# Performance work log

Hardware: AMD Instinct MI355X
Metric: run time of the kernel (lower is better)

## Reference

```python
import jax, jax.numpy as jnp
import numpy as np

N_NODES = 50000
N_EDGES = 800000
D = 128
H = 8
HD = D // H
N_NTYPES = 3
N_ETYPES = 5
LN_EPS = 1e-5


def setup_inputs() -> dict:
    key = jax.random.key(0)
    ks = jax.random.split(key, 16)
    inp = {
        "x": jax.random.normal(ks[0], (N_NODES, D), dtype=jnp.float32),
        "edge_index": jax.random.randint(ks[1], (2, N_EDGES), 0, N_NODES),
        "edge_type": jax.random.randint(ks[2], (N_EDGES,), 0, N_ETYPES),
        "node_type": jax.random.randint(ks[3], (N_NODES,), 0, N_NTYPES),
        # per-(node_type, head) QKV projections, per-(edge_type, head) K transform
        "W_Q": jax.random.normal(ks[4], (N_NTYPES, H, HD, HD), dtype=jnp.float32) * 0.02,
        "W_K": jax.random.normal(ks[5], (N_NTYPES, H, HD, HD), dtype=jnp.float32) * 0.02,
        "W_V": jax.random.normal(ks[6], (N_NTYPES, H, HD, HD), dtype=jnp.float32) * 0.02,
        "W_edge": jax.random.normal(ks[7], (N_ETYPES, H, HD, HD), dtype=jnp.float32) * 0.02,
        "mu": jnp.ones((H, N_ETYPES), dtype=jnp.float32),
        "W_out": jax.random.normal(ks[8], (D, D), dtype=jnp.float32) * 0.02,
        "b_out": jnp.zeros((D,), dtype=jnp.float32),
        "ln1_g": jnp.ones((D,), dtype=jnp.float32),
        "ln1_b": jnp.zeros((D,), dtype=jnp.float32),
        "W1": jax.random.normal(ks[9], (D, 4 * D), dtype=jnp.float32) * 0.02,
        "b1": jnp.zeros((4 * D,), dtype=jnp.float32),
        "W2": jax.random.normal(ks[10], (4 * D, D), dtype=jnp.float32) * 0.02,
        "b2": jnp.zeros((D,), dtype=jnp.float32),
        "ln2_g": jnp.ones((D,), dtype=jnp.float32),
        "ln2_b": jnp.zeros((D,), dtype=jnp.float32),
    }
    return inp


def _layer_norm(y, g, b):
    m = y.mean(-1, keepdims=True)
    v = ((y - m) ** 2).mean(-1, keepdims=True)
    return (y - m) * jax.lax.rsqrt(v + LN_EPS) * g + b


def reference(x, edge_index, edge_type, node_type,
              W_Q, W_K, W_V, W_edge, mu,
              W_out, b_out, ln1_g, ln1_b, W1, b1, W2, b2, ln2_g, ln2_b):
    N = x.shape[0]
    xh = x.reshape(N, H, HD)  # heads vectorized (concat of per-head slices)

    # type-specific QKV: small fixed loop over node types, masked select
    Q = jnp.zeros_like(xh)
    K = jnp.zeros_like(xh)
    V = jnp.zeros_like(xh)
    for t in range(N_NTYPES):
        m = (node_type == t)[:, None, None]
        Q = jnp.where(m, jnp.einsum('nhd,hdf->nhf', xh, W_Q[t]), Q)
        K = jnp.where(m, jnp.einsum('nhd,hdf->nhf', xh, W_K[t]), K)
        V = jnp.where(m, jnp.einsum('nhd,hdf->nhf', xh, W_V[t]), V)

    src, dst = edge_index[0], edge_index[1]
    q_dst = Q[dst]   # [E,H,HD]
    k_src = K[src]   # [E,H,HD]

    # edge-type-specific K transform
    kt = jnp.zeros_like(k_src)
    for et in range(N_ETYPES):
        m = (edge_type == et)[:, None, None]
        kt = jnp.where(m, jnp.einsum('ehd,hdf->ehf', k_src, W_edge[et]), kt)

    scores = (q_dst * kt).sum(-1) / jnp.sqrt(jnp.float32(HD))  # [E,H]
    scores = scores * mu[:, edge_type].T                       # mu per edge type, per head

    # sparse softmax over incoming edges of each dst node, per head
    smax = jax.ops.segment_max(scores, dst, num_segments=N)
    ex = jnp.exp(scores - smax[dst])
    den = jax.ops.segment_sum(ex, dst, num_segments=N)
    w = ex / (den[dst] + 1e-10)                                 # [E,H]

    agg = jax.ops.segment_sum(V[src] * w[..., None], dst, num_segments=N)  # [N,H,HD]
    mh = agg.reshape(N, D) @ W_out + b_out  # dropout is identity in eval

    h = _layer_norm(x + mh, ln1_g, ln1_b)
    ffn = jax.nn.gelu(h @ W1 + b1, approximate=False) @ W2 + b2
    return _layer_norm(h + ffn, ln2_g, ln2_b)
```

## Files before the change

### kernel.cpp

```cpp
#include <hip/hip_runtime.h>
#include <hip/hip_bf16.h>

#define N_NODESC 50000
#define N_EDGESC 800000
#define DD 128
#define HH 8
#define HDIM 16
#define N_NT 3
#define N_ET 5
#define NPB 196
#define NEB 400
#define NFB 512

#define KV8_OFF    ((size_t)0)
#define QT8_OFF    ((size_t)12800000)
#define XP_OFF     ((size_t)44800000)
#define AGG_OFF    ((size_t)57600000)
#define WOUTT_OFF  ((size_t)83200000)
#define W1T_OFF    ((size_t)83232768)
#define W2T_OFF    ((size_t)83363840)
#define WALL_OFF   ((size_t)83494912)
#define EDATA_OFF  ((size_t)84183040)
#define ROWS_OFF   ((size_t)87383040)
#define ORIG_OFF   ((size_t)87583104)
#define DEG_OFF    ((size_t)87783104)
#define TOFS_OFF   ((size_t)87983104)
#define BH_OFF     ((size_t)87983168)
#define BB_OFF     ((size_t)87985536)
#define TMP_OFF    ((size_t)87988928)
#define RLOC_OFF   ((size_t)91188928)
#define CSUM_OFF   ((size_t)91389056)

using short8 = __attribute__((ext_vector_type(8))) short;
using f32x4  = __attribute__((ext_vector_type(4))) float;
using f32x2  = __attribute__((ext_vector_type(2))) float;

__device__ __forceinline__ ushort f2b(float f) {
    __hip_bfloat16 h = __float2bfloat16(f);
    return *(ushort*)&h;
}
__device__ __forceinline__ float b2f(ushort u) {
    __hip_bfloat16 h = *(__hip_bfloat16*)&u;
    return __bfloat162float(h);
}
__device__ __forceinline__ f32x2 pk0(unsigned int w) {
    return __builtin_amdgcn_cvt_pk_f32_fp8((int)w, false);
}
__device__ __forceinline__ f32x2 pk1(unsigned int w) {
    return __builtin_amdgcn_cvt_pk_f32_fp8((int)w, true);
}
__device__ __forceinline__ float gelu_f(float v) {
    const float x = v * 0.70710678118654752f;
    const float ax = fabsf(x);
    const float d = fmaf(0.3275911f, ax, 1.0f);
    float t;
    asm("v_rcp_f32 %0, %1" : "=v"(t) : "v"(d));
    float p = fmaf(1.061405429f, t, -1.453152027f);
    p = fmaf(p, t, 1.421413741f);
    p = fmaf(p, t, -0.284496736f);
    p = fmaf(p, t, 0.254829592f);
    p = p * t;
    const float e = __expf(-ax * ax);
    const float er = 1.0f - p * e;
    const float erfx = (x < 0.f) ? -er : er;
    return 0.5f * v * (1.0f + erfx);
}
__device__ __forceinline__ void ebar() {
    __builtin_amdgcn_sched_barrier(0);
    asm volatile("s_waitcnt lgkmcnt(0)" ::: "memory");
    __builtin_amdgcn_sched_barrier(0);
    __builtin_amdgcn_s_barrier();
    __builtin_amdgcn_sched_barrier(0);
}

__global__ __launch_bounds__(256) void prep_a(
    const float* __restrict__ Wout, const float* __restrict__ W1, const float* __restrict__ W2,
    const float* __restrict__ WQ, const float* __restrict__ Wk, const float* __restrict__ Wv,
    const float* __restrict__ We, const float* __restrict__ mu,
    ushort* __restrict__ Woutt, ushort* __restrict__ W1t, ushort* __restrict__ W2t,
    ushort* __restrict__ Wall,
    const int* __restrict__ ntype, int* __restrict__ bh,
    const int* __restrict__ dst, int* __restrict__ deg, unsigned int* __restrict__ tmp)
{
    const int b = blockIdx.x, tid = threadIdx.x;
    if (b < 1920) {
        const int gid = b * 256 + tid;
        if (gid < 16384) {
            const int nn = gid >> 7, k = gid & 127;
            Woutt[gid] = f2b(Wout[k * 128 + nn]);
        } else if (gid < 81920) {
            const int i = gid - 16384;
            const int nn = i >> 7, k = i & 127;
            W1t[i] = f2b(W1[k * 512 + nn]);
        } else if (gid < 147456) {
            const int i = gid - 81920;
            const int nn = i >> 9, k = i & 511;
            W2t[i] = f2b(W2[k * 128 + nn]);
        } else {
            const int idx = gid - 147456;
            const int t = idx / (896 * 128);
            const int rem = idx % (896 * 128);
            const int c = rem / 128, k = rem % 128;
            const int hk = k >> 4, ck = k & 15;
            float v = 0.f;
            if (c < 128) {
                const int hc = c >> 4, j = c & 15;
                if (hk == hc) v = 4.f * Wk[((t * HH + hc) * HDIM + ck) * HDIM + j];
            } else if (c < 256) {
                const int c2 = c - 128, hc = c2 >> 4, j = c2 & 15;
                if (hk == hc) v = 4.f * Wv[((t * HH + hc) * HDIM + ck) * HDIM + j];
            } else {
                const int cq = c - 256, et = cq >> 7, dd = cq & 127;
                const int hq = dd >> 4, j = dd & 15;
                if (hk == hq) {
                    const float* wq = WQ + ((t * HH + hq) * HDIM + ck) * HDIM;
                    const float* we = We + ((et * HH + hq) * HDIM + j) * HDIM;
                    float s = 0.f;
#pragma unroll
                    for (int f = 0; f < 16; f++) s = fmaf(wq[f], we[f], s);
                    v = 64.f * mu[hq * N_ET + et] * s;
                }
            }
            Wall[idx] = f2b(v);
        }
    } else if (b < 1920 + NPB) {
        const int bc = b - 1920;
        const int wave = tid >> 6, lane = tid & 63;
        const int n = bc * 256 + tid;
        const int t = (n < N_NODESC) ? ntype[n] : -1;
        const unsigned long long m0 = __ballot(t == 0);
        const unsigned long long m1 = __ballot(t == 1);
        const unsigned long long m2 = __ballot(t == 2);
        __shared__ int wcnt[4][3];
        if (lane == 0) {
            wcnt[wave][0] = (int)__popcll(m0);
            wcnt[wave][1] = (int)__popcll(m1);
            wcnt[wave][2] = (int)__popcll(m2);
        }
        __syncthreads();
        if (tid < 3)
            bh[tid * NPB + bc] = wcnt[0][tid] + wcnt[1][tid] + wcnt[2][tid] + wcnt[3][tid];
    } else {
        for (int e = (b - 1920 - NPB) * 256 + tid; e < N_EDGESC; e += NEB * 256) {
            const int nd = dst[e];
            const unsigned int p = (unsigned int)atomicAdd(&deg[nd], 1);
            tmp[e] = (p << 16) | (unsigned int)nd;
        }
    }
}

__global__ __launch_bounds__(256) void prep_b(
    const int* __restrict__ bh, const int* __restrict__ deg,
    int* __restrict__ bb, int* __restrict__ tofs,
    int* __restrict__ rloc, int* __restrict__ csum)
{
    __shared__ int part[256];
    const int tid = threadIdx.x;
    if (blockIdx.x == 0) {
        const int base3 = tid * 3;
        int e0 = (base3 + 0 < 588) ? bh[base3 + 0] : 0;
        int e1 = (base3 + 1 < 588) ? bh[base3 + 1] : 0;
        int e2 = (base3 + 2 < 588) ? bh[base3 + 2] : 0;
        const int l0 = e0, l1 = e0 + e1, l2 = l1 + e2;
        part[tid] = l2;
        __syncthreads();
        for (int off = 1; off < 256; off <<= 1) {
            const int u = (tid >= off) ? part[tid - off] : 0;
            __syncthreads();
            part[tid] += u;
            __syncthreads();
        }
        const int tb = part[tid] - l2;
        if (base3 + 0 < 588) bb[base3 + 0] = tb;
        if (base3 + 1 < 588) bb[base3 + 1] = tb + l0;
        if (base3 + 2 < 588) bb[base3 + 2] = tb + l1;
        __syncthreads();
        if (tid == 0) {
            tofs[0] = 0;
            tofs[1] = bb[NPB];
            tofs[2] = bb[2 * NPB];
            tofs[3] = N_NODESC;
        }
    } else {
        const int c = blockIdx.x - 1;
        const int n = c * 256 + tid;
        const int vdeg = (n < N_NODESC) ? deg[n] : 0;
        part[tid] = vdeg;
        __syncthreads();
        for (int off = 1; off < 256; off <<= 1) {
            const int u = (tid >= off) ? part[tid - off] : 0;
            __syncthreads();
            part[tid] += u;
            __syncthreads();
        }
        if (n <= N_NODESC) rloc[n] = part[tid] - vdeg;
        if (tid == 255) csum[c] = part[255];
    }
}

__global__ __launch_bounds__(256) void prep_c(
    const int* __restrict__ ntype, const float* __restrict__ x,
    const int* __restrict__ src, const int* __restrict__ etype,
    const int* __restrict__ bb, const int* __restrict__ rloc, const int* __restrict__ csum,
    const unsigned int* __restrict__ tmp,
    int* __restrict__ origof, ushort* __restrict__ Xp, int* __restrict__ rows,
    int* __restrict__ edata)
{
    const int b = blockIdx.x, tid = threadIdx.x;
    __shared__ int cb[256];
    {
        const int v = (tid < NPB) ? csum[tid] : 0;
        cb[tid] = v;
        __syncthreads();
        for (int off = 1; off < 256; off <<= 1) {
            const int u = (tid >= off) ? cb[tid - off] : 0;
            __syncthreads();
            cb[tid] += u;
            __syncthreads();
        }
        const int incl = cb[tid];
        __syncthreads();
        cb[tid] = incl - v;
        __syncthreads();
    }

    if (b < NPB) {
        const int wave = tid >> 6, lane = tid & 63;
        const int n = b * 256 + tid;
        const int t = (n < N_NODESC) ? ntype[n] : -1;
        const unsigned long long m0 = __ballot(t == 0);
        const unsigned long long m1 = __ballot(t == 1);
        const unsigned long long m2 = __ballot(t == 2);
        __shared__ int wcnt[4][3];
        __shared__ int sp[256];
        if (lane == 0) {
            wcnt[wave][0] = (int)__popcll(m0);
            wcnt[wave][1] = (int)__popcll(m1);
            wcnt[wave][2] = (int)__popcll(m2);
        }
        __syncthreads();
        int p = -1;
        if (n < N_NODESC) {
            int basew = 0;
#pragma unroll
            for (int w = 0; w < 4; w++) if (w < wave) basew += wcnt[w][t];
            const unsigned long long mt = (t == 0) ? m0 : (t == 1) ? m1 : m2;
            const unsigned long long mlt = ((unsigned long long)1 << lane) - 1;
            p = bb[t * NPB + b] + basew + (int)__popcll(mt & mlt);
            origof[p] = n;
        }
        if (n <= N_NODESC) rows[n] = cb[b] + rloc[n];
        sp[tid] = p;
        __syncthreads();
        for (int i = tid; i < 256 * 16; i += 256) {
            const int nn = i >> 4, c = (i & 15) << 3;
            const int pp = sp[nn];
            if (pp < 0) continue;
            const int n2 = b * 256 + nn;
            const float4 v0 = *(const float4*)(x + (size_t)n2 * DD + c);
            const float4 v1 = *(const float4*)(x + (size_t)n2 * DD + c + 4);
            ushort o[8] = {f2b(v0.x), f2b(v0.y), f2b(v0.z), f2b(v0.w),
                           f2b(v1.x), f2b(v1.y), f2b(v1.z), f2b(v1.w)};
            *(uint4*)(Xp + (size_t)pp * DD + c) = *(uint4*)o;
        }
    } else {
        for (int e = (b - NPB) * 256 + tid; e < N_EDGESC; e += NFB * 256) {
            const unsigned int v = tmp[e];
            const int nd = (int)(v & 0xffffu);
            const int p = (int)(v >> 16);
            edata[cb[nd >> 8] + rloc[nd] + p] = src[e] | (etype[e] << 16);
        }
    }
}

#define LDP 36

__global__ __launch_bounds__(256) void proj_gemm(
    const ushort* __restrict__ Xp, const ushort* __restrict__ Wall,
    const int* __restrict__ tofs, const int* __restrict__ origof,
    ushort* __restrict__ KV8, unsigned char* __restrict__ Qt8)
{
    const int t = blockIdx.z;
    const int rs = tofs[t], re = tofs[t + 1];
    const int mBase = rs + blockIdx.x * 128;
    if (mBase >= re) return;
    const int nBase = blockIdx.y * 128;
    const ushort* Bt = Wall + (size_t)t * 896 * 128;

    __shared__ ushort As[128 * LDP];
    __shared__ ushort Bs[128 * LDP];
    const int tid = threadIdx.x;
    const int lane = tid & 63, wave = tid >> 6;
    const int mw = (wave >> 1) * 64, nw = (wave & 1) * 64;
    const int l15 = lane & 15, q8 = (lane >> 4) * 8;

    f32x4 acc[4][4];
#pragma unroll
    for (int i = 0; i < 4; i++)
#pragma unroll
        for (int j = 0; j < 4; j++) acc[i][j] = (f32x4){0.f, 0.f, 0.f, 0.f};

    const int r0 = tid >> 2, c0 = (tid & 3) * 8;
    int rA0 = mBase + r0;      if (rA0 >= N_NODESC) rA0 = N_NODESC - 1;
    int rA1 = mBase + r0 + 64; if (rA1 >= N_NODESC) rA1 = N_NODESC - 1;

    for (int kk = 0; kk < 128; kk += 32) {
        short8 a0 = *(const short8*)(Xp + (size_t)rA0 * DD + kk + c0);
        short8 a1 = *(const short8*)(Xp + (size_t)rA1 * DD + kk + c0);
        short8 b0 = *(const short8*)(Bt + (size_t)(nBase + r0) * 128 + kk + c0);
        short8 b1 = *(const short8*)(Bt + (size_t)(nBase + r0 + 64) * 128 + kk + c0);
        *(short8*)&As[r0 * LDP + c0] = a0;
        *(short8*)&As[(r0 + 64) * LDP + c0] = a1;
        *(short8*)&Bs[r0 * LDP + c0] = b0;
        *(short8*)&Bs[(r0 + 64) * LDP + c0] = b1;
        __syncthreads();
        short8 af[4], bf[4];
#pragma unroll
        for (int i = 0; i < 4; i++)
            af[i] = *(const short8*)&As[(mw + i * 16 + l15) * LDP + q8];
#pragma unroll
        for (int j = 0; j < 4; j++)
            bf[j] = *(const short8*)&Bs[(nw + j * 16 + l15) * LDP + q8];
#pragma unroll
        for (int i = 0; i < 4; i++)
#pragma unroll
            for (int j = 0; j < 4; j++)
                acc[i][j] = __builtin_amdgcn_mfma_f32_16x16x32_bf16(af[i], bf[j], acc[i][j], 0, 0, 0);
        __syncthreads();
    }

    unsigned char* kvb = (unsigned char*)KV8;
    const int rq = (lane >> 4) * 4;
#pragma unroll
    for (int i = 0; i < 4; i++) {
#pragma unroll
        for (int r = 0; r < 4; r++) {
            const int gm = mBase + mw + i * 16 + rq + r;
            if (gm >= re) continue;
            const int og = origof[gm];
#pragma unroll
            for (int j = 0; j < 4; j++) {
                const int gn = nBase + nw + j * 16 + l15;
                const float v = acc[i][j][r];
                const unsigned char b8 =
                    (unsigned char)(__builtin_amdgcn_cvt_pk_fp8_f32(v, v, 0, false) & 0xff);
                if (gn < 256) kvb[(size_t)og * 256 + gn] = b8;
                else          Qt8[(size_t)og * 640 + (gn - 256)] = b8;
            }
        }
    }
}

__global__ __launch_bounds__(128) void edgeagg_kernel(
    const int* __restrict__ rowstart, const int* __restrict__ edata,
    const unsigned char* __restrict__ Qt8, const unsigned char* __restrict__ KV8,
    ushort* __restrict__ agg)
{
    const int w = threadIdx.x >> 6;
    const int lane = threadIdx.x & 63;
    const int n = blockIdx.x * 2 + w;
    const int slot = lane >> 3;
    const int h = lane & 7;

    __shared__ uint4 qs8s[2][40];
    if (lane < 40)
        qs8s[w][lane] = ((const uint4*)(Qt8 + (size_t)n * 640))[lane];
    __syncthreads();
    const uint* qbase = (const uint*)&qs8s[w][0];

    const int s0 = rowstart[n], s1 = rowstart[n + 1];
    const float qsc = 1.44269504f / 1024.f;

    float acc[16];
#pragma unroll
    for (int j = 0; j < 16; j++) acc[j] = 0.f;
    float den = 0.f;

    for (int i = s0 + slot; i < s1; i += 8) {
        const int ed = edata[i];
        const int sn = ed & 0xffff;
        const int et = ed >> 16;
        const unsigned char* kvp = KV8 + ((size_t)sn << 8);
        const uint4 kw = *(const uint4*)(kvp + (h << 4));
        const uint4 vw = *(const uint4*)(kvp + 128 + (h << 4));
        const uint4 qw = *(const uint4*)(qbase + (et << 5) + (h << 2));

        const f32x2 q0 = pk0(qw.x), q1 = pk1(qw.x), q2 = pk0(qw.y), q3 = pk1(qw.y);
        const f32x2 q4 = pk0(qw.z), q5 = pk1(qw.z), q6 = pk0(qw.w), q7 = pk1(qw.w);
        const f32x2 k0 = pk0(kw.x), k1 = pk1(kw.x), k2 = pk0(kw.y), k3 = pk1(kw.y);
        const f32x2 k4 = pk0(kw.z), k5 = pk1(kw.z), k6 = pk0(kw.w), k7 = pk1(kw.w);

        float pa = q0.x * k0.x;
        float pb = q0.y * k0.y;
        float pc = q1.x * k1.x;
        float pd = q1.y * k1.y;
        pa = fmaf(q2.x, k2.x, pa); pb = fmaf(q2.y, k2.y, pb);
        pc = fmaf(q3.x, k3.x, pc); pd = fmaf(q3.y, k3.y, pd);
        pa = fmaf(q4.x, k4.x, pa); pb = fmaf(q4.y, k4.y, pb);
        pc = fmaf(q5.x, k5.x, pc); pd = fmaf(q5.y, k5.y, pd);
        pa = fmaf(q6.x, k6.x, pa); pb = fmaf(q6.y, k6.y, pb);
        pc = fmaf(q7.x, k7.x, pc); pd = fmaf(q7.y, k7.y, pd);

        const float ex = exp2f(((pa + pb) + (pc + pd)) * qsc);
        den += ex;

        const f32x2 v0 = pk0(vw.x), v1 = pk1(vw.x), v2 = pk0(vw.y), v3 = pk1(vw.y);
        const f32x2 v4 = pk0(vw.z), v5 = pk1(vw.z), v6 = pk0(vw.w), v7 = pk1(vw.w);
        acc[0]  = fmaf(ex, v0.x, acc[0]);  acc[1]  = fmaf(ex, v0.y, acc[1]);
        acc[2]  = fmaf(ex, v1.x, acc[2]);  acc[3]  = fmaf(ex, v1.y, acc[3]);
        acc[4]  = fmaf(ex, v2.x, acc[4]);  acc[5]  = fmaf(ex, v2.y, acc[5]);
        acc[6]  = fmaf(ex, v3.x, acc[6]);  acc[7]  = fmaf(ex, v3.y, acc[7]);
        acc[8]  = fmaf(ex, v4.x, acc[8]);  acc[9]  = fmaf(ex, v4.y, acc[9]);
        acc[10] = fmaf(ex, v5.x, acc[10]); acc[11] = fmaf(ex, v5.y, acc[11]);
        acc[12] = fmaf(ex, v6.x, acc[12]); acc[13] = fmaf(ex, v6.y, acc[13]);
        acc[14] = fmaf(ex, v7.x, acc[14]); acc[15] = fmaf(ex, v7.y, acc[15]);
    }

    {
        const int b0 = slot & 1, b1 = slot & 2, b2 = slot & 4;
#pragma unroll
        for (int j = 0; j < 8; j++) {
            const float v = b0 ? acc[j] : acc[j + 8];
            const float r = __shfl_xor(v, 8);
            acc[j] = (b0 ? acc[j + 8] : acc[j]) + r;
        }
#pragma unroll
        for (int j = 0; j < 4; j++) {
            const float v = b1 ? acc[j] : acc[j + 4];
            const float r = __shfl_xor(v, 16);
            acc[j] = (b1 ? acc[j + 4] : acc[j]) + r;
        }
#pragma unroll
        for (int j = 0; j < 2; j++) {
            const float v = b2 ? acc[j] : acc[j + 2];
            const float r = __shfl_xor(v, 32);
            acc[j] = (b2 ? acc[j + 2] : acc[j]) + r;
        }
        den += __shfl_xor(den, 8);
        den += __shfl_xor(den, 16);
        den += __shfl_xor(den, 32);
    }
    const float rr = 0.25f / (den + 1e-10f);
    const int fb = (h << 4) + ((slot & 1) << 3) + ((slot & 2) << 1) + ((slot & 4) >> 1);
    ushort o2[2] = { f2b(acc[0] * rr), f2b(acc[1] * rr) };
    *(uint*)&agg[((size_t)n << 7) + fb] = *(uint*)o2;
}

#define LDH 132
#define LDB2 68

#define LOADB(P0, P1, PTR) { P0 = *(const short8*)(PTR); P1 = *(const short8*)((PTR) + 8); }
#define STAGEB(BUF, P0, P1) { *(short8*)&Bs[BUF][br * LDB2 + bc] = P0; \
                              *(short8*)&Bs[BUF][br * LDB2 + bc + 8] = P1; }

__global__ __launch_bounds__(512, 4) void fused_tail(
    const ushort* __restrict__ agg, const ushort* __restrict__ Woutt,
    const ushort* __restrict__ W1t, const ushort* __restrict__ W2t,
    const float* __restrict__ x,
    const float* __restrict__ bout, const float* __restrict__ g1, const float* __restrict__ b1ln,
    const float* __restrict__ b1, const float* __restrict__ b2,
    const float* __restrict__ g2, const float* __restrict__ b2ln,
    float* __restrict__ out)
{
    __shared__ ushort Bs[2][128 * LDB2];
    __shared__ ushort Hs[64 * LDH];
    __shared__ ushort Ts[64 * LDH];
    __shared__ float red[2][4][64];

    const int tid = threadIdx.x;
    const int lane = tid & 63, wave = tid >> 6;
    const int wm = wave >> 2, wn = wave & 3;
    const int l15 = lane & 15, q8 = (lane >> 4) * 8, rq = (lane >> 4) * 4;
    const int mBase = blockIdx.x * 64;

    const int br = tid >> 2, bc = (tid & 3) * 16;
    const int ar = tid >> 3, ac = (tid & 7) * 16;
    int rowA = mBase + ar; if (rowA >= N_NODESC) rowA = N_NODESC - 1;

    f32x4 acc1[2][2], acc2[2][2];
#pragma unroll
    for (int i = 0; i < 2; i++)
#pragma unroll
        for (int j = 0; j < 2; j++) {
            acc1[i][j] = (f32x4){0.f, 0.f, 0.f, 0.f};
            acc2[i][j] = (f32x4){0.f, 0.f, 0.f, 0.f};
        }

    short8 pX0, pX1, pY0, pY1, aT0, aT1;
    LOADB(pX0, pX1, Woutt + (size_t)br * 128 + bc);
    LOADB(pY0, pY1, Woutt + (size_t)br * 128 + 64 + bc);
    aT0 = *(const short8*)(agg + (size_t)rowA * DD + ac);
    aT1 = *(const short8*)(agg + (size_t)rowA * DD + ac + 8);
    float xv[2][4][2];
#pragma unroll
    for (int i = 0; i < 2; i++)
#pragma unroll
        for (int r = 0; r < 4; r++) {
            const int gm = mBase + wm * 32 + i * 16 + rq + r;
            const int gr = (gm < N_NODESC) ? gm : N_NODESC - 1;
#pragma unroll
            for (int j = 0; j < 2; j++)
                xv[i][r][j] = x[(size_t)gr * DD + wn * 32 + j * 16 + l15];
        }
    *(short8*)&Ts[ar * LDH + ac] = aT0;
    *(short8*)&Ts[ar * LDH + ac + 8] = aT1;
    STAGEB(0, pX0, pX1);
    LOADB(pX0, pX1, W1t + (size_t)br * 128 + bc);
    ebar();

    STAGEB(1, pY0, pY1);
    LOADB(pY0, pY1, W1t + (size_t)br * 128 + 64 + bc);
#pragma unroll
    for (int kk2 = 0; kk2 < 2; kk2++) {
        short8 af[2], bf[2];
#pragma unroll
        for (int i = 0; i < 2; i++)
            af[i] = *(const short8*)&Ts[(wm * 32 + i * 16 + l15) * LDH + kk2 * 32 + q8];
#pragma unroll
        for (int j = 0; j < 2; j++)
            bf[j] = *(const short8*)&Bs[0][(wn * 32 + j * 16 + l15) * LDB2 + kk2 * 32 + q8];
#pragma unroll
        for (int i = 0; i < 2; i++)
#pragma unroll
            for (int j = 0; j < 2; j++)
                acc1[i][j] = __builtin_amdgcn_mfma_f32_16x16x32_bf16(af[i], bf[j], acc1[i][j], 0, 0, 0);
    }
    ebar();

    STAGEB(0, pX0, pX1);
    LOADB(pX0, pX1, W2t + (size_t)br * 512 + bc);
#pragma unroll
    for (int kk2 = 0; kk2 < 2; kk2++) {
        short8 af[2], bf[2];
#pragma unroll
        for (int i = 0; i < 2; i++)
            af[i] = *(const short8*)&Ts[(wm * 32 + i * 16 + l15) * LDH + 64 + kk2 * 32 + q8];
#pragma unroll
        for (int j = 0; j < 2; j++)
            bf[j] = *(const short8*)&Bs[1][(wn * 32 + j * 16 + l15) * LDB2 + kk2 * 32 + q8];
#pragma unroll
        for (int i = 0; i < 2; i++)
#pragma unroll
            for (int j = 0; j < 2; j++)
                acc1[i][j] = __builtin_amdgcn_mfma_f32_16x16x32_bf16(af[i], bf[j], acc1[i][j], 0, 0, 0);
    }
    ebar();

    {
        float bo[2], gv[2], bv[2];
#pragma unroll
        for (int j = 0; j < 2; j++) {
            const int gn = wn * 32 + j * 16 + l15;
            bo[j] = bout[gn]; gv[j] = g1[gn]; bv[j] = b1ln[gn];
        }
#pragma unroll
        for (int i = 0; i < 2; i++) {
#pragma unroll
            for (int r = 0; r < 4; r++) {
                const int row = wm * 32 + i * 16 + rq + r;
                float s = 0.f, ss = 0.f;
#pragma unroll
                for (int j = 0; j < 2; j++) {
                    float v = acc1[i][j][r] + bo[j] + xv[i][r][j];
                    acc1[i][j][r] = v;
                    s += v; ss += v * v;
                }
                s  += __shfl_xor(s, 1);  s  += __shfl_xor(s, 2);  s  += __shfl_xor(s, 4);  s  += __shfl_xor(s, 8);
                ss += __shfl_xor(ss, 1); ss += __shfl_xor(ss, 2); ss += __shfl_xor(ss, 4); ss += __shfl_xor(ss, 8);
                if (l15 == 0) { red[0][wn][row] = s; red[1][wn][row] = ss; }
            }
        }
        ebar();
#pragma unroll
        for (int i = 0; i < 2; i++) {
#pragma unroll
            for (int r = 0; r < 4; r++) {
                const int row = wm * 32 + i * 16 + rq + r;
                const float s  = red[0][0][row] + red[0][1][row] + red[0][2][row] + red[0][3][row];
                const float ss = red[1][0][row] + red[1][1][row] + red[1][2][row] + red[1][3][row];
                const float mean = s * (1.f / 128.f);
                const float var  = ss * (1.f / 128.f) - mean * mean;
                const float rstd = rsqrtf(var + 1e-5f);
#pragma unroll
                for (int j = 0; j < 2; j++) {
                    const int gn = wn * 32 + j * 16 + l15;
                    Hs[row * LDH + gn] = f2b((acc1[i][j][r] - mean) * rstd * gv[j] + bv[j]);
                }
            }
// ... 102 lines not shown
                for (int j = 0; j < 2; j++)
                    acc2[i][j] = __builtin_amdgcn_mfma_f32_16x16x32_bf16(af[i], bf[j], acc2[i][j], 0, 0, 0);
        }
        ebar();
    }

    {
        float b2v[2], gv[2], bv[2];
#pragma unroll
        for (int j = 0; j < 2; j++) {
            const int gn = wn * 32 + j * 16 + l15;
            b2v[j] = b2[gn]; gv[j] = g2[gn]; bv[j] = b2ln[gn];
        }
#pragma unroll
        for (int i = 0; i < 2; i++) {
#pragma unroll
            for (int r = 0; r < 4; r++) {
                const int row = wm * 32 + i * 16 + rq + r;
                float s = 0.f, ss = 0.f;
#pragma unroll
                for (int j = 0; j < 2; j++) {
                    const int gn = wn * 32 + j * 16 + l15;
                    float v = acc2[i][j][r] + b2v[j] + b2f(Hs[row * LDH + gn]);
                    acc2[i][j][r] = v;
                    s += v; ss += v * v;
                }
                s  += __shfl_xor(s, 1);  s  += __shfl_xor(s, 2);  s  += __shfl_xor(s, 4);  s  += __shfl_xor(s, 8);
                ss += __shfl_xor(ss, 1); ss += __shfl_xor(ss, 2); ss += __shfl_xor(ss, 4); ss += __shfl_xor(ss, 8);
                if (l15 == 0) { red[0][wn][row] = s; red[1][wn][row] = ss; }
            }
        }
        ebar();
#pragma unroll
        for (int i = 0; i < 2; i++) {
#pragma unroll
            for (int r = 0; r < 4; r++) {
                const int row = wm * 32 + i * 16 + rq + r;
                const int gm = mBase + row;
                if (gm >= N_NODESC) continue;
                const float s  = red[0][0][row] + red[0][1][row] + red[0][2][row] + red[0][3][row];
                const float ss = red[1][0][row] + red[1][1][row] + red[1][2][row] + red[1][3][row];
                const float mean = s * (1.f / 128.f);
                const float var  = ss * (1.f / 128.f) - mean * mean;
                const float rstd = rsqrtf(var + 1e-5f);
#pragma unroll
                for (int j = 0; j < 2; j++) {
                    const int gn = wn * 32 + j * 16 + l15;
                    out[(size_t)gm * DD + gn] = (acc2[i][j][r] - mean) * rstd * gv[j] + bv[j];
                }
            }
        }
    }
}

extern "C" void kernel_launch(void* const* d_in, const int* in_sizes, int n_in,
                              void* d_out, int out_size, void* d_ws, size_t ws_size,
                              hipStream_t stream)
{
    const float* x     = (const float*)d_in[0];
    const int*   ei    = (const int*)d_in[1];
    const int*   etyp  = (const int*)d_in[2];
    const int*   ntype = (const int*)d_in[3];
    const float* Wq    = (const float*)d_in[4];
    const float* Wk    = (const float*)d_in[5];
    const float* Wv    = (const float*)d_in[6];
    const float* We    = (const float*)d_in[7];
    const float* mu    = (const float*)d_in[8];
    const float* Wout  = (const float*)d_in[9];
    const float* bout  = (const float*)d_in[10];
    const float* g1    = (const float*)d_in[11];
    const float* b1ln  = (const float*)d_in[12];
    const float* W1    = (const float*)d_in[13];
    const float* b1    = (const float*)d_in[14];
    const float* W2    = (const float*)d_in[15];
    const float* b2    = (const float*)d_in[16];
    const float* g2    = (const float*)d_in[17];
    const float* b2ln  = (const float*)d_in[18];
    float* out = (float*)d_out;

    char* ws = (char*)d_ws;
    ushort*        KV8   = (ushort*)(ws + KV8_OFF);
    unsigned char* Qt8   = (unsigned char*)(ws + QT8_OFF);
    ushort*        Xp    = (ushort*)(ws + XP_OFF);
    ushort*        agg   = (ushort*)(ws + AGG_OFF);
    ushort*        Woutt = (ushort*)(ws + WOUTT_OFF);
    ushort*        W1t   = (ushort*)(ws + W1T_OFF);
    ushort*        W2t   = (ushort*)(ws + W2T_OFF);
    ushort*        Wall  = (ushort*)(ws + WALL_OFF);
    int*           edata = (int*)(ws + EDATA_OFF);
    int*           rows  = (int*)(ws + ROWS_OFF);
    int*           origof= (int*)(ws + ORIG_OFF);
    int*           deg   = (int*)(ws + DEG_OFF);
    int*           tofs  = (int*)(ws + TOFS_OFF);
    int*           bh    = (int*)(ws + BH_OFF);
    int*           bb    = (int*)(ws + BB_OFF);
    unsigned int*  tmp   = (unsigned int*)(ws + TMP_OFF);
    int*           rloc  = (int*)(ws + RLOC_OFF);
    int*           csum  = (int*)(ws + CSUM_OFF);

    const int* srcA = ei;
    const int* dstA = ei + N_EDGESC;

    (void)hipMemsetAsync(ws + DEG_OFF, 0, 200000, stream);

    prep_a<<<1920 + NPB + NEB, 256, 0, stream>>>(
        Wout, W1, W2, Wq, Wk, Wv, We, mu, Woutt, W1t, W2t, Wall,
        ntype, bh, dstA, deg, tmp);
    prep_b<<<1 + NPB, 256, 0, stream>>>(bh, deg, bb, tofs, rloc, csum);
    prep_c<<<NPB + NFB, 256, 0, stream>>>(ntype, x, srcA, etyp, bb, rloc, csum, tmp,
                                          origof, Xp, rows, edata);

    proj_gemm<<<dim3(394, 7, 3), 256, 0, stream>>>(Xp, Wall, tofs, origof, KV8, Qt8);
    edgeagg_kernel<<<N_NODESC / 2, 128, 0, stream>>>(rows, edata, Qt8,
                                                     (const unsigned char*)KV8, agg);

    fused_tail<<<782, 512, 0, stream>>>(agg, Woutt, W1t, W2t, x,
                                        bout, g1, b1ln, b1, b2, g2, b2ln, out);
}
```

Measured before the change: 322.3 us.

## Fuse edge attention aggregation into the tail GEMM kernel

Removes the separate edge aggregation kernel and performs the per-node sparse softmax aggregation inside fused_tail. Each wave processes 8 consecutive nodes, double-buffering their Q vectors in shared memory, and writes the aggregated result straight into the shared A tile. This drops the global round trip for agg and one kernel launch. In exchange, each wave handles nodes serially inside a block sized for the GEMM (782 blocks), so gather parallelism and latency hiding may drop compared with the 25000-block standalone kernel.

```diff
diff --git a/kernel.cpp b/kernel.cpp
--- a/kernel.cpp
+++ b/kernel.cpp
@@ -15,7 +15,6 @@
 #define KV8_OFF    ((size_t)0)
 #define QT8_OFF    ((size_t)12800000)
 #define XP_OFF     ((size_t)44800000)
-#define AGG_OFF    ((size_t)57600000)
 #define WOUTT_OFF  ((size_t)83200000)
 #define W1T_OFF    ((size_t)83232768)
 #define W2T_OFF    ((size_t)83363840)
@@ -351,101 +350,6 @@
     }
 }
 
-__global__ __launch_bounds__(128) void edgeagg_kernel(
-    const int* __restrict__ rowstart, const int* __restrict__ edata,
-    const unsigned char* __restrict__ Qt8, const unsigned char* __restrict__ KV8,
-    ushort* __restrict__ agg)
-{
-    const int w = threadIdx.x >> 6;
-    const int lane = threadIdx.x & 63;
-    const int n = blockIdx.x * 2 + w;
-    const int slot = lane >> 3;
-    const int h = lane & 7;
-
-    __shared__ uint4 qs8s[2][40];
-    if (lane < 40)
-        qs8s[w][lane] = ((const uint4*)(Qt8 + (size_t)n * 640))[lane];
-    __syncthreads();
-    const uint* qbase = (const uint*)&qs8s[w][0];
-
-    const int s0 = rowstart[n], s1 = rowstart[n + 1];
-    const float qsc = 1.44269504f / 1024.f;
-
-    float acc[16];
-#pragma unroll
-    for (int j = 0; j < 16; j++) acc[j] = 0.f;
-    float den = 0.f;
-
-    for (int i = s0 + slot; i < s1; i += 8) {
-        const int ed = edata[i];
-        const int sn = ed & 0xffff;
-        const int et = ed >> 16;
-        const unsigned char* kvp = KV8 + ((size_t)sn << 8);
-        const uint4 kw = *(const uint4*)(kvp + (h << 4));
-        const uint4 vw = *(const uint4*)(kvp + 128 + (h << 4));
-        const uint4 qw = *(const uint4*)(qbase + (et << 5) + (h << 2));
-
-        const f32x2 q0 = pk0(qw.x), q1 = pk1(qw.x), q2 = pk0(qw.y), q3 = pk1(qw.y);
-        const f32x2 q4 = pk0(qw.z), q5 = pk1(qw.z), q6 = pk0(qw.w), q7 = pk1(qw.w);
-        const f32x2 k0 = pk0(kw.x), k1 = pk1(kw.x), k2 = pk0(kw.y), k3 = pk1(kw.y);
-        const f32x2 k4 = pk0(kw.z), k5 = pk1(kw.z), k6 = pk0(kw.w), k7 = pk1(kw.w);
-
-        float pa = q0.x * k0.x;
-        float pb = q0.y * k0.y;
-        float pc = q1.x * k1.x;
-        float pd = q1.y * k1.y;
-        pa = fmaf(q2.x, k2.x, pa); pb = fmaf(q2.y, k2.y, pb);
-        pc = fmaf(q3.x, k3.x, pc); pd = fmaf(q3.y, k3.y, pd);
-        pa = fmaf(q4.x, k4.x, pa); pb = fmaf(q4.y, k4.y, pb);
-        pc = fmaf(q5.x, k5.x, pc); pd = fmaf(q5.y, k5.y, pd);
-        pa = fmaf(q6.x, k6.x, pa); pb = fmaf(q6.y, k6.y, pb);
-        pc = fmaf(q7.x, k7.x, pc); pd = fmaf(q7.y, k7.y, pd);
-
-        const float ex = exp2f(((pa + pb) + (pc + pd)) * qsc);
-        den += ex;
-
-        const f32x2 v0 = pk0(vw.x), v1 = pk1(vw.x), v2 = pk0(vw.y), v3 = pk1(vw.y);
-        const f32x2 v4 = pk0(vw.z), v5 = pk1(vw.z), v6 = pk0(vw.w), v7 = pk1(vw.w);
-        acc[0]  = fmaf(ex, v0.x, acc[0]);  acc[1]  = fmaf(ex, v0.y, acc[1]);
-        acc[2]  = fmaf(ex, v1.x, acc[2]);  acc[3]  = fmaf(ex, v1.y, acc[3]);
-        acc[4]  = fmaf(ex, v2.x, acc[4]);  acc[5]  = fmaf(ex, v2.y, acc[5]);
-        acc[6]  = fmaf(ex, v3.x, acc[6]);  acc[7]  = fmaf(ex, v3.y, acc[7]);
-        acc[8]  = fmaf(ex, v4.x, acc[8]);  acc[9]  = fmaf(ex, v4.y, acc[9]);
-        acc[10] = fmaf(ex, v5.x, acc[10]); acc[11] = fmaf(ex, v5.y, acc[11]);
-        acc[12] = fmaf(ex, v6.x, acc[12]); acc[13] = fmaf(ex, v6.y, acc[13]);
-        acc[14] = fmaf(ex, v7.x, acc[14]); acc[15] = fmaf(ex, v7.y, acc[15]);
-    }
-
-    {
-        const int b0 = slot & 1, b1 = slot & 2, b2 = slot & 4;
-#pragma unroll
-        for (int j = 0; j < 8; j++) {
-            const float v = b0 ? acc[j] : acc[j + 8];
-            const float r = __shfl_xor(v, 8);
-            acc[j] = (b0 ? acc[j + 8] : acc[j]) + r;
-        }
-#pragma unroll
-        for (int j = 0; j < 4; j++) {
-            const float v = b1 ? acc[j] : acc[j + 4];
-            const float r = __shfl_xor(v, 16);
-            acc[j] = (b1 ? acc[j + 4] : acc[j]) + r;
-        }
-#pragma unroll
-        for (int j = 0; j < 2; j++) {
-            const float v = b2 ? acc[j] : acc[j + 2];
-            const float r = __shfl_xor(v, 32);
-            acc[j] = (b2 ? acc[j + 2] : acc[j]) + r;
-        }
-        den += __shfl_xor(den, 8);
-        den += __shfl_xor(den, 16);
-        den += __shfl_xor(den, 32);
-    }
-    const float rr = 0.25f / (den + 1e-10f);
-    const int fb = (h << 4) + ((slot & 1) << 3) + ((slot & 2) << 1) + ((slot & 4) >> 1);
-    ushort o2[2] = { f2b(acc[0] * rr), f2b(acc[1] * rr) };
-    *(uint*)&agg[((size_t)n << 7) + fb] = *(uint*)o2;
-}
-
 #define LDH 132
 #define LDB2 68
 
@@ -454,17 +358,19 @@
                               *(short8*)&Bs[BUF][br * LDB2 + bc + 8] = P1; }
 
 __global__ __launch_bounds__(512, 4) void fused_tail(
-    const ushort* __restrict__ agg, const ushort* __restrict__ Woutt,
-    const ushort* __restrict__ W1t, const ushort* __restrict__ W2t,
+    const int* __restrict__ rows, const int* __restrict__ edata,
+    const unsigned char* __restrict__ Qt8, const unsigned char* __restrict__ KV8,
+    const ushort* __restrict__ Woutt, const ushort* __restrict__ W1t,
+    const ushort* __restrict__ W2t,
     const float* __restrict__ x,
     const float* __restrict__ bout, const float* __restrict__ g1, const float* __restrict__ b1ln,
     const float* __restrict__ b1, const float* __restrict__ b2,
     const float* __restrict__ g2, const float* __restrict__ b2ln,
     float* __restrict__ out)
 {
-    __shared__ ushort Bs[2][128 * LDB2];
-    __shared__ ushort Hs[64 * LDH];
-    __shared__ ushort Ts[64 * LDH];
+    __shared__ __align__(16) ushort Bs[2][128 * LDB2];
+    __shared__ __align__(16) ushort Hs[64 * LDH];
+    __shared__ __align__(16) ushort Ts[64 * LDH];
     __shared__ float red[2][4][64];
 
     const int tid = threadIdx.x;
@@ -474,8 +380,120 @@
     const int mBase = blockIdx.x * 64;
 
     const int br = tid >> 2, bc = (tid & 3) * 16;
-    const int ar = tid >> 3, ac = (tid & 7) * 16;
-    int rowA = mBase + ar; if (rowA >= N_NODESC) rowA = N_NODESC - 1;
+
+    short8 pX0, pX1, pY0, pY1;
+    LOADB(pX0, pX1, Woutt + (size_t)br * 128 + bc);
+    LOADB(pY0, pY1, Woutt + (size_t)br * 128 + 64 + bc);
+    float xv[2][4][2];
+#pragma unroll
+    for (int i = 0; i < 2; i++)
+#pragma unroll
+        for (int r = 0; r < 4; r++) {
+            const int gm = mBase + wm * 32 + i * 16 + rq + r;
+            const int gr = (gm < N_NODESC) ? gm : N_NODESC - 1;
+#pragma unroll
+            for (int j = 0; j < 2; j++)
+                xv[i][r][j] = x[(size_t)gr * DD + wn * 32 + j * 16 + l15];
+        }
+
+    {
+        const int slot = lane >> 3;
+        const int h = lane & 7;
+        uint* Hqu = (uint*)Hs;
+        const int qbA = wave * 320, qbB = qbA + 160;
+        {
+            const int nd0 = mBase + wave * 8;
+            if (lane < 40 && nd0 < N_NODESC)
+                *(uint4*)&Hqu[qbA + lane * 4] =
+                    ((const uint4*)(Qt8 + (size_t)nd0 * 640))[lane];
+        }
+        const float qsc = 1.44269504f / 1024.f;
+        for (int q = 0; q < 8; q++) {
+            const int nd = mBase + wave * 8 + q;
+            uint4 nq = make_uint4(0u, 0u, 0u, 0u);
+            if (q < 7 && lane < 40 && nd + 1 < N_NODESC)
+                nq = ((const uint4*)(Qt8 + (size_t)(nd + 1) * 640))[lane];
+            if (nd < N_NODESC) {
+                const uint* qbase = &Hqu[(q & 1) ? qbB : qbA];
+                const int s0 = rows[nd], s1 = rows[nd + 1];
+                float acc[16];
+#pragma unroll
+                for (int j = 0; j < 16; j++) acc[j] = 0.f;
+                float den = 0.f;
+                for (int i = s0 + slot; i < s1; i += 8) {
+                    const int ed = edata[i];
+                    const int sn = ed & 0xffff;
+                    const int et = ed >> 16;
+                    const unsigned char* kvp = KV8 + ((size_t)sn << 8);
+                    const uint4 kw = *(const uint4*)(kvp + (h << 4));
+                    const uint4 vw = *(const uint4*)(kvp + 128 + (h << 4));
+                    const uint4 qw = *(const uint4*)(qbase + (et << 5) + (h << 2));
+
+                    const f32x2 q0 = pk0(qw.x), q1 = pk1(qw.x), q2 = pk0(qw.y), q3 = pk1(qw.y);
+                    const f32x2 q4 = pk0(qw.z), q5 = pk1(qw.z), q6 = pk0(qw.w), q7 = pk1(qw.w);
+                    const f32x2 k0 = pk0(kw.x), k1 = pk1(kw.x), k2 = pk0(kw.y), k3 = pk1(kw.y);
+                    const f32x2 k4 = pk0(kw.z), k5 = pk1(kw.z), k6 = pk0(kw.w), k7 = pk1(kw.w);
+
+                    float pa = q0.x * k0.x;
+                    float pb = q0.y * k0.y;
+                    float pc = q1.x * k1.x;
+                    float pd = q1.y * k1.y;
+                    pa = fmaf(q2.x, k2.x, pa); pb = fmaf(q2.y, k2.y, pb);
+                    pc = fmaf(q3.x, k3.x, pc); pd = fmaf(q3.y, k3.y, pd);
+                    pa = fmaf(q4.x, k4.x, pa); pb = fmaf(q4.y, k4.y, pb);
+                    pc = fmaf(q5.x, k5.x, pc); pd = fmaf(q5.y, k5.y, pd);
+                    pa = fmaf(q6.x, k6.x, pa); pb = fmaf(q6.y, k6.y, pb);
+                    pc = fmaf(q7.x, k7.x, pc); pd = fmaf(q7.y, k7.y, pd);
+
+                    const float ex = exp2f(((pa + pb) + (pc + pd)) * qsc);
+                    den += ex;
+
+                    const f32x2 v0 = pk0(vw.x), v1 = pk1(vw.x), v2 = pk0(vw.y), v3 = pk1(vw.y);
+                    const f32x2 v4 = pk0(vw.z), v5 = pk1(vw.z), v6 = pk0(vw.w), v7 = pk1(vw.w);
+                    acc[0]  = fmaf(ex, v0.x, acc[0]);  acc[1]  = fmaf(ex, v0.y, acc[1]);
+                    acc[2]  = fmaf(ex, v1.x, acc[2]);  acc[3]  = fmaf(ex, v1.y, acc[3]);
+                    acc[4]  = fmaf(ex, v2.x, acc[4]);  acc[5]  = fmaf(ex, v2.y, acc[5]);
+                    acc[6]  = fmaf(ex, v3.x, acc[6]);  acc[7]  = fmaf(ex, v3.y, acc[7]);
+                    acc[8]  = fmaf(ex, v4.x, acc[8]);  acc[9]  = fmaf(ex, v4.y, acc[9]);
+                    acc[10] = fmaf(ex, v5.x, acc[10]); acc[11] = fmaf(ex, v5.y, acc[11]);
+                    acc[12] = fmaf(ex, v6.x, acc[12]); acc[13] = fmaf(ex, v6.y, acc[13]);
+                    acc[14] = fmaf(ex, v7.x, acc[14]); acc[15] = fmaf(ex, v7.y, acc[15]);
+                }
+                {
+                    const int b0 = slot & 1, b1s = slot & 2, b2s = slot & 4;
+#pragma unroll
+                    for (int j = 0; j < 8; j++) {
+                        const float v = b0 ? acc[j] : acc[j + 8];
+                        const float r = __shfl_xor(v, 8);
+                        acc[j] = (b0 ? acc[j + 8] : acc[j]) + r;
+                    }
+#pragma unroll
+                    for (int j = 0; j < 4; j++) {
+                        const float v = b1s ? acc[j] : acc[j + 4];
+                        const float r = __shfl_xor(v, 16);
+                        acc[j] = (b1s ? acc[j + 4] : acc[j]) + r;
+                    }
+#pragma unroll
+                    for (int j = 0; j < 2; j++) {
+                        const float v = b2s ? acc[j] : acc[j + 2];
+                        const float r = __shfl_xor(v, 32);
+                        acc[j] = (b2s ? acc[j + 2] : acc[j]) + r;
+                    }
+                    den += __shfl_xor(den, 8);
+                    den += __shfl_xor(den, 16);
+                    den += __shfl_xor(den, 32);
+                }
+                const float rr = 0.25f / (den + 1e-10f);
+                const int fb = (h << 4) + ((slot & 1) << 3) + ((slot & 2) << 1) + ((slot & 4) >> 1);
+                const int row = wave * 8 + q;
+                ushort o2[2] = { f2b(acc[0] * rr), f2b(acc[1] * rr) };
+                *(uint*)&Ts[row * LDH + fb] = *(uint*)o2;
+            }
+            if (q < 7 && lane < 40)
+                *(uint4*)&Hqu[((q & 1) ? qbA : qbB) + lane * 4] = nq;
+        }
+    }
+    ebar();
 
     f32x4 acc1[2][2], acc2[2][2];
 #pragma unroll
@@ -486,24 +504,6 @@
             acc2[i][j] = (f32x4){0.f, 0.f, 0.f, 0.f};
         }
 
-    short8 pX0, pX1, pY0, pY1, aT0, aT1;
-    LOADB(pX0, pX1, Woutt + (size_t)br * 128 + bc);
-    LOADB(pY0, pY1, Woutt + (size_t)br * 128 + 64 + bc);
-    aT0 = *(const short8*)(agg + (size_t)rowA * DD + ac);
-    aT1 = *(const short8*)(agg + (size_t)rowA * DD + ac + 8);
-    float xv[2][4][2];
-#pragma unroll
-    for (int i = 0; i < 2; i++)
-#pragma unroll
-        for (int r = 0; r < 4; r++) {
-            const int gm = mBase + wm * 32 + i * 16 + rq + r;
-            const int gr = (gm < N_NODESC) ? gm : N_NODESC - 1;
-#pragma unroll
-            for (int j = 0; j < 2; j++)
-                xv[i][r][j] = x[(size_t)gr * DD + wn * 32 + j * 16 + l15];
-        }
-    *(short8*)&Ts[ar * LDH + ac] = aT0;
-    *(short8*)&Ts[ar * LDH + ac + 8] = aT1;
     STAGEB(0, pX0, pX1);
     LOADB(pX0, pX1, W1t + (size_t)br * 128 + bc);
     ebar();
@@ -772,7 +772,6 @@
     ushort*        KV8   = (ushort*)(ws + KV8_OFF);
     unsigned char* Qt8   = (unsigned char*)(ws + QT8_OFF);
     ushort*        Xp    = (ushort*)(ws + XP_OFF);
-    ushort*        agg   = (ushort*)(ws + AGG_OFF);
     ushort*        Woutt = (ushort*)(ws + WOUTT_OFF);
     ushort*        W1t   = (ushort*)(ws + W1T_OFF);
     ushort*        W2t   = (ushort*)(ws + W2T_OFF);
@@ -801,9 +800,8 @@
                                           origof, Xp, rows, edata);
 
     proj_gemm<<<dim3(394, 7, 3), 256, 0, stream>>>(Xp, Wall, tofs, origof, KV8, Qt8);
-    edgeagg_kernel<<<N_NODESC / 2, 128, 0, stream>>>(rows, edata, Qt8,
-                                                     (const unsigned char*)KV8, agg);
-
-    fused_tail<<<782, 512, 0, stream>>>(agg, Woutt, W1t, W2t, x,
+
+    fused_tail<<<782, 512, 0, stream>>>(rows, edata, Qt8, (const unsigned char*)KV8,
+                                        Woutt, W1t, W2t, x,
                                         bout, g1, b1ln, b1, b2, g2, b2ln, out);
 }
```

Result: slower. 329.5 us (+2.2%).

## Exploit head block-diagonal weights in projection GEMM with pre-swizzled fragments

Applied to the files above, without the earlier changes.

The per-node-type projection weight was a dense 896x128 matrix, mostly zero because each head only mixes its own 16 input dims. The change packs only the nonzero head-pair blocks into a fragment-ordered buffer (28672 entries per type), which shrinks the weight-prep grid. Each GEMM block then loads its whole weight slice into LDS once, for 64 rows, and issues only the non-zero MFMAs, cutting MFMA work and weight traffic by about 4x. The cost is roughly 60KB of LDS per block, which lowers occupancy, and byte-wise scattered global stores that remain uncoalesced.

```diff
diff --git a/kernel.cpp b/kernel.cpp
--- a/kernel.cpp
+++ b/kernel.cpp
@@ -11,6 +11,7 @@
 #define NPB 196
 #define NEB 400
 #define NFB 512
+#define WPB 912
 
 #define KV8_OFF    ((size_t)0)
 #define QT8_OFF    ((size_t)12800000)
@@ -19,7 +20,7 @@
 #define WOUTT_OFF  ((size_t)83200000)
 #define W1T_OFF    ((size_t)83232768)
 #define W2T_OFF    ((size_t)83363840)
-#define WALL_OFF   ((size_t)83494912)
+#define WHPF_OFF   ((size_t)83494912)
 #define EDATA_OFF  ((size_t)84183040)
 #define ROWS_OFF   ((size_t)87383040)
 #define ORIG_OFF   ((size_t)87583104)
@@ -78,12 +79,12 @@
     const float* __restrict__ WQ, const float* __restrict__ Wk, const float* __restrict__ Wv,
     const float* __restrict__ We, const float* __restrict__ mu,
     ushort* __restrict__ Woutt, ushort* __restrict__ W1t, ushort* __restrict__ W2t,
-    ushort* __restrict__ Wall,
+    ushort* __restrict__ Whpf,
     const int* __restrict__ ntype, int* __restrict__ bh,
     const int* __restrict__ dst, int* __restrict__ deg, unsigned int* __restrict__ tmp)
 {
     const int b = blockIdx.x, tid = threadIdx.x;
-    if (b < 1920) {
+    if (b < WPB) {
         const int gid = b * 256 + tid;
         if (gid < 16384) {
             const int nn = gid >> 7, k = gid & 127;
@@ -98,33 +99,38 @@
             W2t[i] = f2b(W2[k * 128 + nn]);
         } else {
             const int idx = gid - 147456;
-            const int t = idx / (896 * 128);
-            const int rem = idx % (896 * 128);
-            const int c = rem / 128, k = rem % 128;
-            const int hk = k >> 4, ck = k & 15;
+            const int t = idx / 28672;
+            const int r = idx % 28672;
+            const int i = r & 7;
+            const int l = (r >> 3) & 63;
+            const int f = r >> 9;
+            const int j = f % 14, p = f / 14;
+            const int c = j * 16 + (l & 15);
+            const int k = ((l >> 4) << 3) + i;
+            const int hi = (c >= 112) ? 1 : 0;
+            const int h = 2 * p + hi;
             float v = 0.f;
-            if (c < 128) {
-                const int hc = c >> 4, j = c & 15;
-                if (hk == hc) v = 4.f * Wk[((t * HH + hc) * HDIM + ck) * HDIM + j];
-            } else if (c < 256) {
-                const int c2 = c - 128, hc = c2 >> 4, j = c2 & 15;
-                if (hk == hc) v = 4.f * Wv[((t * HH + hc) * HDIM + ck) * HDIM + j];
-            } else {
-                const int cq = c - 256, et = cq >> 7, dd = cq & 127;
-                const int hq = dd >> 4, j = dd & 15;
-                if (hk == hq) {
-                    const float* wq = WQ + ((t * HH + hq) * HDIM + ck) * HDIM;
-                    const float* we = We + ((et * HH + hq) * HDIM + j) * HDIM;
+            if ((k >> 4) == hi) {
+                const int kp = k & 15;
+                const int cl = c - hi * 112;
+                if (cl < 16) {
+                    v = 4.f * Wk[((t * HH + h) * HDIM + kp) * HDIM + cl];
+                } else if (cl < 32) {
+                    v = 4.f * Wv[((t * HH + h) * HDIM + kp) * HDIM + (cl - 16)];
+                } else {
+                    const int et = (cl - 32) >> 4, jj = (cl - 32) & 15;
+                    const float* wq = WQ + ((t * HH + h) * HDIM + kp) * HDIM;
+                    const float* we = We + ((et * HH + h) * HDIM + jj) * HDIM;
                     float s = 0.f;
 #pragma unroll
-                    for (int f = 0; f < 16; f++) s = fmaf(wq[f], we[f], s);
-                    v = 64.f * mu[hq * N_ET + et] * s;
+                    for (int ff = 0; ff < 16; ff++) s = fmaf(wq[ff], we[ff], s);
+                    v = 64.f * mu[h * N_ET + et] * s;
                 }
             }
-            Wall[idx] = f2b(v);
-        }
-    } else if (b < 1920 + NPB) {
-        const int bc = b - 1920;
+            Whpf[idx] = f2b(v);
+        }
+    } else if (b < WPB + NPB) {
+        const int bc = b - WPB;
         const int wave = tid >> 6, lane = tid & 63;
         const int n = bc * 256 + tid;
         const int t = (n < N_NODESC) ? ntype[n] : -1;
@@ -141,7 +147,7 @@
         if (tid < 3)
             bh[tid * NPB + bc] = wcnt[0][tid] + wcnt[1][tid] + wcnt[2][tid] + wcnt[3][tid];
     } else {
-        for (int e = (b - 1920 - NPB) * 256 + tid; e < N_EDGESC; e += NEB * 256) {
+        for (int e = (b - WPB - NPB) * 256 + tid; e < N_EDGESC; e += NEB * 256) {
             const int nd = dst[e];
             const unsigned int p = (unsigned int)atomicAdd(&deg[nd], 1);
             tmp[e] = (p << 16) | (unsigned int)nd;
@@ -273,79 +279,68 @@
     }
 }
 
-#define LDP 36
+#define LDX 132
 
 __global__ __launch_bounds__(256) void proj_gemm(
-    const ushort* __restrict__ Xp, const ushort* __restrict__ Wall,
+    const ushort* __restrict__ Xp, const ushort* __restrict__ Whpf,
     const int* __restrict__ tofs, const int* __restrict__ origof,
-    ushort* __restrict__ KV8, unsigned char* __restrict__ Qt8)
+    unsigned char* __restrict__ KV8b, unsigned char* __restrict__ Qt8)
 {
-    const int t = blockIdx.z;
+    const int t = blockIdx.y;
     const int rs = tofs[t], re = tofs[t + 1];
-    const int mBase = rs + blockIdx.x * 128;
+    const int mBase = rs + blockIdx.x * 64;
     if (mBase >= re) return;
-    const int nBase = blockIdx.y * 128;
-    const ushort* Bt = Wall + (size_t)t * 896 * 128;
-
-    __shared__ ushort As[128 * LDP];
-    __shared__ ushort Bs[128 * LDP];
+
+    __shared__ ushort Xs[64 * LDX];
+    __shared__ ushort Ws[28672];
+
     const int tid = threadIdx.x;
     const int lane = tid & 63, wave = tid >> 6;
-    const int mw = (wave >> 1) * 64, nw = (wave & 1) * 64;
-    const int l15 = lane & 15, q8 = (lane >> 4) * 8;
-
-    f32x4 acc[4][4];
-#pragma unroll
-    for (int i = 0; i < 4; i++)
-#pragma unroll
-        for (int j = 0; j < 4; j++) acc[i][j] = (f32x4){0.f, 0.f, 0.f, 0.f};
-
-    const int r0 = tid >> 2, c0 = (tid & 3) * 8;
-    int rA0 = mBase + r0;      if (rA0 >= N_NODESC) rA0 = N_NODESC - 1;
-    int rA1 = mBase + r0 + 64; if (rA1 >= N_NODESC) rA1 = N_NODESC - 1;
-
-    for (int kk = 0; kk < 128; kk += 32) {
-        short8 a0 = *(const short8*)(Xp + (size_t)rA0 * DD + kk + c0);
-        short8 a1 = *(const short8*)(Xp + (size_t)rA1 * DD + kk + c0);
-        short8 b0 = *(const short8*)(Bt + (size_t)(nBase + r0) * 128 + kk + c0);
-        short8 b1 = *(const short8*)(Bt + (size_t)(nBase + r0 + 64) * 128 + kk + c0);
-        *(short8*)&As[r0 * LDP + c0] = a0;
-        *(short8*)&As[(r0 + 64) * LDP + c0] = a1;
-        *(short8*)&Bs[r0 * LDP + c0] = b0;
-        *(short8*)&Bs[(r0 + 64) * LDP + c0] = b1;
-        __syncthreads();
-        short8 af[4], bf[4];
-#pragma unroll
-        for (int i = 0; i < 4; i++)
-            af[i] = *(const short8*)&As[(mw + i * 16 + l15) * LDP + q8];
-#pragma unroll
-        for (int j = 0; j < 4; j++)
-            bf[j] = *(const short8*)&Bs[(nw + j * 16 + l15) * LDP + q8];
-#pragma unroll
-        for (int i = 0; i < 4; i++)
-#pragma unroll
-            for (int j = 0; j < 4; j++)
-                acc[i][j] = __builtin_amdgcn_mfma_f32_16x16x32_bf16(af[i], bf[j], acc[i][j], 0, 0, 0);
-        __syncthreads();
-    }
-
-    unsigned char* kvb = (unsigned char*)KV8;
-    const int rq = (lane >> 4) * 4;
-#pragma unroll
-    for (int i = 0; i < 4; i++) {
-#pragma unroll
-        for (int r = 0; r < 4; r++) {
-            const int gm = mBase + mw + i * 16 + rq + r;
-            if (gm >= re) continue;
-            const int og = origof[gm];
-#pragma unroll
-            for (int j = 0; j < 4; j++) {
-                const int gn = nBase + nw + j * 16 + l15;
-                const float v = acc[i][j][r];
+    const int l15 = lane & 15, rq = (lane >> 4) * 4;
+
+#pragma unroll
+    for (int it = 0; it < 4; it++) {
+        const int idx = it * 256 + tid;
+        const int row = idx >> 4, ch = idx & 15;
+        int gr = mBase + row; if (gr >= N_NODESC) gr = N_NODESC - 1;
+        *(uint4*)&Xs[row * LDX + ch * 8] = *(const uint4*)(Xp + (size_t)gr * DD + ch * 8);
+    }
+    const ushort* Wg = Whpf + (size_t)t * 28672;
+#pragma unroll
+    for (int it = 0; it < 14; it++) {
+        const int idx = it * 256 + tid;
+        *(uint4*)&Ws[idx * 8] = *(const uint4*)(Wg + (size_t)idx * 8);
+    }
+    __syncthreads();
+
+    int ogr[4]; bool vr[4];
+#pragma unroll
+    for (int r = 0; r < 4; r++) {
+        const int gm = mBase + wave * 16 + rq + r;
+        vr[r] = (gm < re);
+        ogr[r] = vr[r] ? origof[gm] : 0;
+    }
+
+    for (int p = 0; p < 4; p++) {
+        const short8 af = *(const short8*)&Xs[(wave * 16 + l15) * LDX + p * 32 + (lane >> 4) * 8];
+#pragma unroll
+        for (int j = 0; j < 14; j++) {
+            const short8 bf = *(const short8*)&Ws[((p * 14 + j) * 64 + lane) * 8];
+            f32x4 c = __builtin_amdgcn_mfma_f32_16x16x32_bf16(
+                af, bf, (f32x4){0.f, 0.f, 0.f, 0.f}, 0, 0, 0);
+            const int hi = (j >= 7) ? 1 : 0;
+            const int h = 2 * p + hi;
+            const int jj = j - hi * 7;
+#pragma unroll
+            for (int r = 0; r < 4; r++) {
+                if (!vr[r]) continue;
+                const float v = c[r];
                 const unsigned char b8 =
                     (unsigned char)(__builtin_amdgcn_cvt_pk_fp8_f32(v, v, 0, false) & 0xff);
-                if (gn < 256) kvb[(size_t)og * 256 + gn] = b8;
-                else          Qt8[(size_t)og * 640 + (gn - 256)] = b8;
+                const size_t og = (size_t)ogr[r];
+                if (jj == 0)      KV8b[og * 256 + h * 16 + l15] = b8;
+                else if (jj == 1) KV8b[og * 256 + 128 + h * 16 + l15] = b8;
+                else              Qt8[og * 640 + (jj - 2) * 128 + h * 16 + l15] = b8;
             }
         }
     }
@@ -776,7 +771,7 @@
     ushort*        Woutt = (ushort*)(ws + WOUTT_OFF);
     ushort*        W1t   = (ushort*)(ws + W1T_OFF);
     ushort*        W2t   = (ushort*)(ws + W2T_OFF);
-    ushort*        Wall  = (ushort*)(ws + WALL_OFF);
+    ushort*        Whpf  = (ushort*)(ws + WHPF_OFF);
     int*           edata = (int*)(ws + EDATA_OFF);
     int*           rows  = (int*)(ws + ROWS_OFF);
     int*           origof= (int*)(ws + ORIG_OFF);
@@ -793,14 +788,15 @@
 
     (void)hipMemsetAsync(ws + DEG_OFF, 0, 200000, stream);
 
-    prep_a<<<1920 + NPB + NEB, 256, 0, stream>>>(
-        Wout, W1, W2, Wq, Wk, Wv, We, mu, Woutt, W1t, W2t, Wall,
+    prep_a<<<WPB + NPB + NEB, 256, 0, stream>>>(
+        Wout, W1, W2, Wq, Wk, Wv, We, mu, Woutt, W1t, W2t, Whpf,
         ntype, bh, dstA, deg, tmp);
     prep_b<<<1 + NPB, 256, 0, stream>>>(bh, deg, bb, tofs, rloc, csum);
     prep_c<<<NPB + NFB, 256, 0, stream>>>(ntype, x, srcA, etyp, bb, rloc, csum, tmp,
                                           origof, Xp, rows, edata);
 
-    proj_gemm<<<dim3(394, 7, 3), 256, 0, stream>>>(Xp, Wall, tofs, origof, KV8, Qt8);
+    proj_gemm<<<dim3(782, 3), 256, 0, stream>>>(Xp, Whpf, tofs, origof,
+                                                (unsigned char*)KV8, Qt8);
     edgeagg_kernel<<<N_NODESC / 2, 128, 0, stream>>>(rows, edata, Qt8,
                                                      (const unsigned char*)KV8, agg);
 
```

Result: faster. 310.3 us (-3.7%).
